# Performance work log

Hardware: AMD Instinct MI355X
Metric: run time of the kernel (lower is better)

## Reference

```python
import jax, jax.numpy as jnp
import numpy as np

PRECISION = 2.0 ** 24  # ctx._precision stand-in; factor = sqrt(precision)
SF_CONST = 48.0


def setup_inputs() -> dict:
    key = jax.random.key(0)
    k1, k2, k3 = jax.random.split(key, 3)
    x = jax.random.normal(k1, (16, 128, 128, 128), dtype=jnp.float32)  # NCHW
    W = jax.random.normal(k2, (256, 128, 3, 3), dtype=jnp.float32) * 0.05  # OIHW
    b = jax.random.normal(k3, (256,), dtype=jnp.float32) * 0.1
    return {"x": x, "W": W, "b": b}


def reference(x, W, b):
    # --- quantize() (standard, non-mixture path) ---
    N = float(np.prod(W.shape[1:]))           # in_ch * kh * kw = 1152
    factor = np.sqrt(PRECISION)               # sqrt(ctx._precision)
    sf = np.sqrt(SF_CONST / N)
    w_sum = jnp.sum(jnp.abs(W), axis=(1, 2, 3))          # [O]
    w_sum = jnp.where(w_sum == 0, 1.0, w_sum)
    fw = (factor / sf - np.sqrt(N / 12.0) * 5.0) / w_sum  # [O]
    Wq = jnp.round(W * fw[:, None, None, None])

    # --- forward int-quantized conv ---
    x_max = jnp.max(jnp.abs(x))
    fx = jnp.where(x_max > 0, (factor * sf - 0.5) / x_max, 1.0)
    xq = jnp.round(fx * x)
    y = jax.lax.conv_general_dilated(
        xq, Wq,
        window_strides=(1, 1),
        padding=((1, 1), (1, 1)),
        dimension_numbers=("NCHW", "OIHW", "NCHW"),
    )
    # dequantize per output channel, then fused float bias add
    y = y / (fx * fw[:, None, None]) + b[:, None, None]
    # Activation (ReLU); BN disabled, dropout disabled in this config
    return jax.nn.relu(y)
```

## Files before the change

### kernel.cpp

```cpp
#include <hip/hip_runtime.h>
#include <math.h>


#define FW_NUM 20017.23017802413f
#define FX_NUM 835.5924988699913f
#define WQA_OFF 2048
#define WQB_OFF (640 * 1024)
#define ZP_OFF  (1536 * 1024)
#define XQ_OFF  (2 * 1024 * 1024)
#define XQ_BYTES 67108864ull

#define CK  16
#define CKP 24
#define JW  130

typedef _Float16 half8 __attribute__((ext_vector_type(8)));
typedef _Float16 half4 __attribute__((ext_vector_type(4)));
typedef float floatx16 __attribute__((ext_vector_type(16)));

__device__ __forceinline__ void gl_lds16(const void* g, void* s) {
    __builtin_amdgcn_global_load_lds((const __attribute__((address_space(1))) void*)g,
                                     (__attribute__((address_space(3))) void*)s, 16, 0, 0);
}

__global__ void xmax_kernel(const float* __restrict__ x, unsigned int* wsu, int n4) {
    int tid = blockIdx.x * blockDim.x + threadIdx.x;
    int stride = gridDim.x * blockDim.x;
    const float4* x4 = (const float4*)x;
    float m = 0.f;
    for (int i = tid; i < n4; i += stride) {
        float4 v = x4[i];
        m = fmaxf(m, fmaxf(fmaxf(fabsf(v.x), fabsf(v.y)), fmaxf(fabsf(v.z), fabsf(v.w))));
    }
    #pragma unroll
    for (int off = 32; off >= 1; off >>= 1)
        m = fmaxf(m, __shfl_down(m, off, 64));
    __shared__ float sm[4];
    if ((threadIdx.x & 63) == 0) sm[threadIdx.x >> 6] = m;
    __syncthreads();
    if (threadIdx.x == 0) {
        m = fmaxf(fmaxf(sm[0], sm[1]), fmaxf(sm[2], sm[3]));
        atomicMax(wsu, __float_as_uint(m));
    }
}

__global__ void wq_kernel(const float* __restrict__ W, float* wsf, int big) {
    int o = blockIdx.x;
    int t = threadIdx.x;
    const float* wrow = W + o * 1152;
    float wv[9];
    float s = 0.f;
    #pragma unroll
    for (int k = 0; k < 9; k++) { wv[k] = wrow[t * 9 + k]; s += fabsf(wv[k]); }
    #pragma unroll
    for (int off = 32; off >= 1; off >>= 1) s += __shfl_down(s, off, 64);
    __shared__ float sred[2];
    __shared__ float sfw;
    if ((t & 63) == 0) sred[t >> 6] = s;
    __syncthreads();
    if (t == 0) {
        float wsum = sred[0] + sred[1];
        if (wsum == 0.f) wsum = 1.f;
        float fw = FW_NUM / wsum;
        wsf[64 + o] = fw;
        sfw = fw;
    }
    __syncthreads();
    float fw = sfw;
    _Float16* wqa = (_Float16*)((char*)wsf + WQA_OFF);
    _Float16* wqb = (_Float16*)((char*)wsf + WQB_OFF);
    #pragma unroll
    for (int k = 0; k < 9; k++) {
        _Float16 hv = (_Float16)rintf(wv[k] * fw);
        wqa[(o * 9 + k) * 128 + t] = hv;
        if (big)
            wqb[(((t >> 4) * 9 + k) * 256 + o) * 16 + (t & 15)] = hv;
    }
}

__global__ void quantx_kernel(const float* __restrict__ x, const float* __restrict__ wsf,
                              _Float16* __restrict__ xq) {
    int bid = blockIdx.x;
    int h  = bid & 127;
    int cc = (bid >> 7) & 7;
    int n  = bid >> 10;
    float xmax = __uint_as_float(((const unsigned int*)wsf)[0]);
    float fx = xmax > 0.f ? FX_NUM / xmax : 1.0f;
    int w = threadIdx.x;
    const float* xp = x + ((size_t)(n * 128 + cc * 16) * 128 + h) * 128 + w;
    half8 v0, v1;
    #pragma unroll
    for (int ci = 0; ci < 8; ci++)  v0[ci] = (_Float16)rintf(fx * xp[(size_t)ci * 16384]);
    #pragma unroll
    for (int ci = 8; ci < 16; ci++) v1[ci - 8] = (_Float16)rintf(fx * xp[(size_t)ci * 16384]);
    _Float16* op = xq + ((size_t)bid * 128 + w) * 16;
    *(half8*)op = v0;
    *(half8*)(op + 8) = v1;
}

__global__ __launch_bounds__(256, 3) void conv_main(const _Float16* __restrict__ xq,
                                                    const float* __restrict__ bias,
                                                    const float* __restrict__ wsf,
                                                    float* __restrict__ out) {
    __shared__ __align__(16) _Float16 xs[2][10240];
    __shared__ float sc[32], bz[32];

    float xmax = __uint_as_float(((const unsigned int*)wsf)[0]);
    float fx = xmax > 0.f ? FX_NUM / xmax : 1.0f;

    int bx0 = blockIdx.x;
    int bx = (bx0 & 7) * 512 + (bx0 >> 3);
    int o0 = (bx & 7) << 5;
    int w0 = ((bx >> 3) & 3) << 5;
    int h0 = ((bx >> 5) & 7) << 4;
    int n  = bx >> 8;

    int tid = threadIdx.x;
    int lane = tid & 63;
    int wv = tid >> 6;
    int m32 = lane & 31;
    int q2 = lane >> 5;

    const char* wsb = (const char*)wsf;

    int goff[5];
    int gstr[5];
    #pragma unroll
    for (int k = 0; k < 5; ++k) {
        int s = wv + 4 * k;
        int slot = s * 64 + lane;
        int r = (slot * 241) >> 14;
        int spi = slot - r * 68;
        int h = h0 + r - 1;
        int w = w0 + (spi >> 1) - 1;
        bool ok = (slot < 1224) && (h >= 0) && (h < 128) && (w >= 0) && (w < 128);
        if (ok) {
            goff[k] = XQ_OFF + n * 4194304 + (h * 128 + w) * 32 + (spi & 1) * 16;
            gstr[k] = 524288;
        } else {
            goff[k] = ZP_OFF + lane * 16;
            gstr[k] = 0;
        }
    }
    auto stage = [&](int tb) {
        #pragma unroll
        for (int k = 0; k < 5; ++k) {
            int s = wv + 4 * k;
            gl_lds16(wsb + goff[k], (char*)&xs[tb][0] + s * 1024);
            goff[k] += gstr[k];
        }
    };

    if (tid < 32) {
        float fwv = wsf[64 + o0 + tid];
        sc[tid] = 1.0f / (fx * fwv);
        bz[tid] = bias[o0 + tid];
    }

    floatx16 acc[4];
    #pragma unroll
    for (int p = 0; p < 4; ++p)
        #pragma unroll
        for (int e = 0; e < 16; ++e) acc[p][e] = 0.f;

    stage(0);

    for (int cc = 0; cc < 8; ++cc) {
        int cb = cc & 1;
        __builtin_amdgcn_s_barrier();
        if (cc < 7) {
            stage(cb ^ 1);
            asm volatile("s_waitcnt vmcnt(5)" ::: "memory");
        } else {
            asm volatile("s_waitcnt vmcnt(0)" ::: "memory");
        }
        __builtin_amdgcn_s_barrier();

        const char* xb = (const char*)&xs[cb][0] + wv * (4 * 1088);
        const char* wq_c = wsb + WQB_OFF + (size_t)cc * 73728 + (o0 + m32) * 32 + q2 * 16;

        half8 wfA[3], wfB[3];
        #pragma unroll
        for (int kh = 0; kh < 3; ++kh)
            wfA[kh] = *(const half8*)(wq_c + (kh * 3 + 0) * 8192);

        #pragma unroll
        for (int kw = 0; kw < 3; ++kw) {
            half8 xf[6];
            #pragma unroll
            for (int srow = 0; srow < 6; ++srow)
                xf[srow] = *(const half8*)(xb + srow * 1088 + (m32 + kw) * 32 + q2 * 16);
            if (kw < 2) {
                #pragma unroll
                for (int kh = 0; kh < 3; ++kh) {
                    if (kw & 1) wfA[kh] = *(const half8*)(wq_c + (kh * 3 + kw + 1) * 8192);
                    else        wfB[kh] = *(const half8*)(wq_c + (kh * 3 + kw + 1) * 8192);
                }
            }
            __builtin_amdgcn_s_setprio(1);
            #pragma unroll
            for (int kh = 0; kh < 3; ++kh) {
                half8 wcur = (kw & 1) ? wfB[kh] : wfA[kh];
                #pragma unroll
                for (int p = 0; p < 4; ++p)
                    acc[p] = __builtin_amdgcn_mfma_f32_32x32x16_f16(wcur, xf[p + kh], acc[p], 0, 0, 0);
            }
            __builtin_amdgcn_s_setprio(0);
        }
    }

    #pragma unroll
    for (int e = 0; e < 16; ++e) {
        int o_loc = (e & 3) + 8 * (e >> 2) + 4 * q2;
        float scale = sc[o_loc];
        float bv = bz[o_loc];
        #pragma unroll
        for (int p = 0; p < 4; ++p) {
            int h = h0 + wv * 4 + p;
            float v = fmaxf(fmaf(acc[p][e], scale, bv), 0.f);
            out[(((size_t)(n * 256 + o0 + o_loc)) * 128 + h) * 128 + w0 + m32] = v;
        }
    }
}

__global__ __launch_bounds__(256, 2) void conv_fallback(const float* __restrict__ x,
                                                        const float* __restrict__ bias,
                                                        const float* __restrict__ wsf,
                                                        float* __restrict__ out) {
    __shared__ __align__(16) _Float16 xs[6 * JW * CKP];
    __shared__ __align__(16) _Float16 wlds[9 * 64 * CKP];

    const unsigned int* wsu = (const unsigned int*)wsf;
    float xmax = __uint_as_float(wsu[0]);
    float fx = xmax > 0.f ? FX_NUM / xmax : 1.0f;

    int bx = blockIdx.x;
    int n  = bx >> 5;
    int h0 = (bx & 31) << 2;
    int o0 = blockIdx.y << 6;

    int tid  = threadIdx.x;
    int lane = tid & 63;
    int wave = tid >> 6;
    int m32  = lane & 31;
    int q2   = lane >> 5;

    const _Float16* wq16 = (const _Float16*)((const char*)wsf + WQA_OFF);
    const float* xn = x + (size_t)n * (128 * 128 * 128);

    floatx16 acc[4][2];
    #pragma unroll
    for (int mt = 0; mt < 4; mt++)
        #pragma unroll
        for (int nt = 0; nt < 2; nt++)
            #pragma unroll
            for (int e = 0; e < 16; e++) acc[mt][nt][e] = 0.f;

    if (tid < 192) {
        int r = tid >> 5;
        int s = tid & 31;
        int c = s & 15;
        int j = (s >> 4) ? (JW - 1) : 0;
        xs[(r * JW + j) * CKP + c] = (_Float16)0.f;
    }

    for (int c0 = 0; c0 < 128; c0 += CK) {
        __syncthreads();
        #pragma unroll
        for (int it = 0; it < 12; ++it) {
            int idx = tid + it * 256;
            int j  = (idx & 127) + 1;
            int c4 = (idx >> 7) & 3;
            int r  = idx >> 9;
            int h  = h0 + r - 1;
            float v0 = 0.f, v1 = 0.f, v2 = 0.f, v3 = 0.f;
            if (h >= 0 && h < 128) {
                const float* xp = xn + (size_t)(c0 + c4 * 4) * 16384 + h * 128 + (j - 1);
                v0 = xp[0]; v1 = xp[16384]; v2 = xp[32768]; v3 = xp[49152];
            }
            half4 hv;
            hv[0] = (_Float16)rintf(fx * v0);
            hv[1] = (_Float16)rintf(fx * v1);
            hv[2] = (_Float16)rintf(fx * v2);
            hv[3] = (_Float16)rintf(fx * v3);
            *(half4*)&xs[(r * JW + j) * CKP + c4 * 4] = hv;
        }
        #pragma unroll
        for (int it = 0; it < 5; ++it) {
            int idx = tid + it * 256;
            if (idx < 1152) {
                int o   = idx / 18;
                int rem = idx - o * 18;
                int tap = rem >> 1;
                int g   = rem & 1;
                half8 v = *(const half8*)(wq16 + ((size_t)(o0 + o) * 9 + tap) * 128 + c0 + g * 8);
                *(half8*)&wlds[(tap * 64 + o) * CKP + g * 8] = v;
            }
        }
        __syncthreads();

        const _Float16* xbase = &xs[(wave * JW + m32) * CKP + q2 * 8];
        const _Float16* wbase = &wlds[m32 * CKP + q2 * 8];
        #pragma unroll
        for (int kh = 0; kh < 3; ++kh) {
            #pragma unroll
            for (int kw = 0; kw < 3; ++kw) {
                int tap = kh * 3 + kw;
                half8 b0 = *(const half8*)(wbase + (tap * 64 +  0) * CKP);
                half8 b1 = *(const half8*)(wbase + (tap * 64 + 32) * CKP);
                #pragma unroll
                for (int mt = 0; mt < 4; ++mt) {
                    half8 a = *(const half8*)(xbase + (kh * JW + kw + mt * 32) * CKP);
                    acc[mt][0] = __builtin_amdgcn_mfma_f32_32x32x16_f16(a, b0, acc[mt][0], 0, 0, 0);
                    acc[mt][1] = __builtin_amdgcn_mfma_f32_32x32x16_f16(a, b1, acc[mt][1], 0, 0, 0);
                }
            }
        }
    }

    int h = h0 + wave;
    #pragma unroll
    for (int nt = 0; nt < 2; ++nt) {
        int o = o0 + nt * 32 + m32;
        float fwv = wsf[64 + o];
        float scale = 1.0f / (fx * fwv);
        float bv = bias[o];
        float* op = out + (((size_t)n * 256 + o) * 128 + h) * 128;
        #pragma unroll
        for (int mt = 0; mt < 4; ++mt) {
            #pragma unroll
            for (int g = 0; g < 4; ++g) {
                int w = mt * 32 + 8 * g + 4 * q2;
                float4 r;
                r.x = fmaxf(fmaf(acc[mt][nt][4 * g + 0], scale, bv), 0.f);
                r.y = fmaxf(fmaf(acc[mt][nt][4 * g + 1], scale, bv), 0.f);
                r.z = fmaxf(fmaf(acc[mt][nt][4 * g + 2], scale, bv), 0.f);
                r.w = fmaxf(fmaf(acc[mt][nt][4 * g + 3], scale, bv), 0.f);
                *(float4*)(op + w) = r;
            }
        }
    }
}

extern "C" void kernel_launch(void* const* d_in, const int* in_sizes, int n_in,
                              void* d_out, int out_size, void* d_ws, size_t ws_size,
                              hipStream_t stream) {
    const float* x = (const float*)d_in[0];
    const float* W = (const float*)d_in[1];
    const float* b = (const float*)d_in[2];
    float* out = (float*)d_out;
    float* wsf = (float*)d_ws;

    int big = (ws_size >= (size_t)XQ_OFF + XQ_BYTES) ? 1 : 0;

    hipMemsetAsync(d_ws, 0, 256, stream);
    if (big)
        hipMemsetAsync((char*)d_ws + ZP_OFF, 0, 2048, stream);

    xmax_kernel<<<1024, 256, 0, stream>>>(x, (unsigned int*)d_ws, (16 * 128 * 128 * 128) / 4);
    wq_kernel<<<256, 128, 0, stream>>>(W, wsf, big);

    if (big) {
        _Float16* xq = (_Float16*)((char*)d_ws + XQ_OFF);
        quantx_kernel<<<16 * 8 * 128, 128, 0, stream>>>(x, wsf, xq);
        conv_main<<<4096, 256, 0, stream>>>(xq, b, wsf, out);
    } else {
        dim3 grid(512, 4);
        conv_fallback<<<grid, 256, 0, stream>>>(x, b, wsf, out);
    }
}
```

Baseline: 509.6 us.

## Stage weights through LDS and deepen input pipeline to triple buffering

Weights are now staged into LDS with async global-to-LDS loads, double buffered per channel chunk, so the per-thread global weight loads inside the MFMA loop go away. The input tile buffer grows from two to three stages so loads are issued two chunks ahead, with adjusted vmcnt waits. The channel loop is fully unrolled and a sched_barrier is added. In exchange, LDS use rises and launch bounds drop from 3 to 2 blocks per SIMD, which may lower occupancy.

```diff
diff --git a/kernel.cpp b/kernel.cpp
--- a/kernel.cpp
+++ b/kernel.cpp
@@ -98,11 +98,13 @@
     *(half8*)(op + 8) = v1;
 }
 
-__global__ __launch_bounds__(256, 3) void conv_main(const _Float16* __restrict__ xq,
+__global__ __launch_bounds__(256, 2) void conv_main(const _Float16* __restrict__ xq,
                                                     const float* __restrict__ bias,
                                                     const float* __restrict__ wsf,
                                                     float* __restrict__ out) {
-    __shared__ __align__(16) _Float16 xs[2][10240];
+    __shared__ __align__(16) _Float16 xs[3][10240];
+    __shared__ __align__(16) _Float16 wl[2][4608];
+    __shared__ __align__(16) _Float16 wdump[512];
     __shared__ float sc[32], bz[32];
 
     float xmax = __uint_as_float(((const unsigned int*)wsf)[0]);
@@ -123,8 +125,8 @@
 
     const char* wsb = (const char*)wsf;
 
-    int goff[5];
-    int gstr[5];
+    int xoff[5];
+    int xstr[5];
     #pragma unroll
     for (int k = 0; k < 5; ++k) {
         int s = wv + 4 * k;
@@ -135,19 +137,42 @@
         int w = w0 + (spi >> 1) - 1;
         bool ok = (slot < 1224) && (h >= 0) && (h < 128) && (w >= 0) && (w < 128);
         if (ok) {
-            goff[k] = XQ_OFF + n * 4194304 + (h * 128 + w) * 32 + (spi & 1) * 16;
-            gstr[k] = 524288;
+            xoff[k] = XQ_OFF + n * 4194304 + (h * 128 + w) * 32 + (spi & 1) * 16;
+            xstr[k] = 524288;
         } else {
-            goff[k] = ZP_OFF + lane * 16;
-            gstr[k] = 0;
-        }
-    }
-    auto stage = [&](int tb) {
+            xoff[k] = ZP_OFF + lane * 16;
+            xstr[k] = 0;
+        }
+    }
+    int woff[3];
+    int wstr[3];
+    #pragma unroll
+    for (int k = 0; k < 3; ++k) {
+        int t = wv + 4 * k;
+        if (t < 9) {
+            woff[k] = WQB_OFF + t * 8192 + o0 * 32 + lane * 16;
+            wstr[k] = 73728;
+        } else {
+            woff[k] = ZP_OFF + lane * 16;
+            wstr[k] = 0;
+        }
+    }
+
+    auto stage_x = [&](int tb) {
         #pragma unroll
         for (int k = 0; k < 5; ++k) {
             int s = wv + 4 * k;
-            gl_lds16(wsb + goff[k], (char*)&xs[tb][0] + s * 1024);
-            goff[k] += gstr[k];
+            gl_lds16(wsb + xoff[k], (char*)&xs[tb][0] + s * 1024);
+            xoff[k] += xstr[k];
+        }
+    };
+    auto stage_w = [&](int tb) {
+        #pragma unroll
+        for (int k = 0; k < 3; ++k) {
+            int t = wv + 4 * k;
+            char* dst = (t < 9) ? ((char*)&wl[tb][0] + t * 1024) : (char*)&wdump[0];
+            gl_lds16(wsb + woff[k], dst);
+            woff[k] += wstr[k];
         }
     };
 
@@ -163,47 +188,39 @@
         #pragma unroll
         for (int e = 0; e < 16; ++e) acc[p][e] = 0.f;
 
-    stage(0);
-
+    stage_w(0);
+    stage_x(0);
+    stage_x(1);
+
+    #pragma unroll
     for (int cc = 0; cc < 8; ++cc) {
-        int cb = cc & 1;
         __builtin_amdgcn_s_barrier();
-        if (cc < 7) {
-            stage(cb ^ 1);
-            asm volatile("s_waitcnt vmcnt(5)" ::: "memory");
-        } else {
-            asm volatile("s_waitcnt vmcnt(0)" ::: "memory");
-        }
+        if (cc < 7) stage_w((cc + 1) & 1);
+        if (cc < 6) stage_x((cc + 2) % 3);
+        if (cc < 6)       asm volatile("s_waitcnt vmcnt(13)" ::: "memory");
+        else if (cc == 6) asm volatile("s_waitcnt vmcnt(8)" ::: "memory");
+        else              asm volatile("s_waitcnt vmcnt(0)" ::: "memory");
         __builtin_amdgcn_s_barrier();
-
-        const char* xb = (const char*)&xs[cb][0] + wv * (4 * 1088);
-        const char* wq_c = wsb + WQB_OFF + (size_t)cc * 73728 + (o0 + m32) * 32 + q2 * 16;
-
-        half8 wfA[3], wfB[3];
-        #pragma unroll
-        for (int kh = 0; kh < 3; ++kh)
-            wfA[kh] = *(const half8*)(wq_c + (kh * 3 + 0) * 8192);
-
+        __builtin_amdgcn_sched_barrier(0);
+
+        const char* xb = (const char*)&xs[cc % 3][0] + wv * (4 * 1088);
+        const char* wb = (const char*)&wl[cc & 1][0];
         #pragma unroll
         for (int kw = 0; kw < 3; ++kw) {
             half8 xf[6];
             #pragma unroll
             for (int srow = 0; srow < 6; ++srow)
                 xf[srow] = *(const half8*)(xb + srow * 1088 + (m32 + kw) * 32 + q2 * 16);
-            if (kw < 2) {
-                #pragma unroll
-                for (int kh = 0; kh < 3; ++kh) {
-                    if (kw & 1) wfA[kh] = *(const half8*)(wq_c + (kh * 3 + kw + 1) * 8192);
-                    else        wfB[kh] = *(const half8*)(wq_c + (kh * 3 + kw + 1) * 8192);
-                }
-            }
+            half8 wf[3];
+            #pragma unroll
+            for (int kh = 0; kh < 3; ++kh)
+                wf[kh] = *(const half8*)(wb + (kh * 3 + kw) * 1024 + m32 * 32 + q2 * 16);
             __builtin_amdgcn_s_setprio(1);
             #pragma unroll
             for (int kh = 0; kh < 3; ++kh) {
-                half8 wcur = (kw & 1) ? wfB[kh] : wfA[kh];
                 #pragma unroll
                 for (int p = 0; p < 4; ++p)
-                    acc[p] = __builtin_amdgcn_mfma_f32_32x32x16_f16(wcur, xf[p + kh], acc[p], 0, 0, 0);
+                    acc[p] = __builtin_amdgcn_mfma_f32_32x32x16_f16(wf[kh], xf[p + kh], acc[p], 0, 0, 0);
             }
             __builtin_amdgcn_s_setprio(0);
         }
```

Result: no change. 511.9 us (+0.5%).
